# Kernel optimization log

Hardware: AMD Instinct MI355X
Metric: run time of the kernel (lower is better)

Reference implementation:

```python
import jax, jax.numpy as jnp
import numpy as np

EMBED = 1024
HEADS = 16
HEAD_DIM = EMBED // HEADS


def _rope(t):
    # t: (B, S, H, D) -> rotary embedding applied over last dim (GPT-NeoX rotate-half)
    B, S, H, D = t.shape
    half = D // 2
    inv_freq = 1.0 / (10000.0 ** (jnp.arange(0, half, dtype=jnp.float32) / half))
    freqs = jnp.arange(S, dtype=jnp.float32)[:, None] * inv_freq[None, :]  # (S, half)
    cos = jnp.cos(freqs)[None, :, None, :]
    sin = jnp.sin(freqs)[None, :, None, :]
    t1, t2 = t[..., :half], t[..., half:]
    return jnp.concatenate([t1 * cos - t2 * sin, t2 * cos + t1 * sin], axis=-1)


def setup_inputs() -> dict:
    key = jax.random.key(0)
    k1, k2, k3 = jax.random.split(key, 3)
    B, S = 2, 2048
    x = jax.random.normal(k1, (B, S, EMBED), dtype=jnp.float32)
    attn_mask = jnp.ones((B, S), dtype=bool)
    w_qkv = jax.random.normal(k2, (EMBED, 3 * EMBED), dtype=jnp.float32) * (1.0 / np.sqrt(EMBED))
    w_out = jax.random.normal(k3, (EMBED, EMBED), dtype=jnp.float32) * (1.0 / np.sqrt(EMBED))
    return {"x": x, "attn_mask": attn_mask, "w_qkv": w_qkv, "w_out": w_out, "is_causal": 1}


def reference(x, attn_mask, w_qkv, w_out, is_causal):
    B, S, E = x.shape
    qkv = x @ w_qkv                                   # (B, S, 3E)
    q, k, v = jnp.split(qkv, 3, axis=-1)
    q = q.reshape(B, S, HEADS, HEAD_DIM)
    k = k.reshape(B, S, HEADS, HEAD_DIM)
    v = v.reshape(B, S, HEADS, HEAD_DIM)
    q = _rope(q)
    k = _rope(k)
    scale = 1.0 / np.sqrt(HEAD_DIM)
    scores = jnp.einsum('bqhd,bkhd->bhqk', q, k) * scale  # (B, H, S, S)
    neg = jnp.asarray(-1e30, dtype=scores.dtype)
    if is_causal:
        causal = jnp.tril(jnp.ones((S, S), dtype=bool))
        scores = jnp.where(causal[None, None], scores, neg)
    else:
        scores = jnp.where(attn_mask[:, None, None, :], scores, neg)
    attn = jax.nn.softmax(scores, axis=-1)
    y = jnp.einsum('bhqk,bkhd->bqhd', attn, v).reshape(B, S, E)
    return y @ w_out
```

## Files before the change

kernel.cpp:

```cpp
#include <hip/hip_runtime.h>
#include <hip/hip_bf16.h>
#include <stdint.h>

typedef float v4f __attribute__((ext_vector_type(4)));
typedef short v8s __attribute__((ext_vector_type(8)));

#define LOG2E 1.44269504088896f
#define QSCALE (0.125f * LOG2E)
#define SOFTMAX_OFF 16.0f

__device__ __forceinline__ unsigned short f2bf(float f) {
    unsigned int u = __float_as_uint(f);
    u += 0x7fffu + ((u >> 16) & 1u);
    return (unsigned short)(u >> 16);
}

#define LDS_FENCE() __builtin_amdgcn_fence(__ATOMIC_ACQ_REL, "workgroup")

__device__ __forceinline__ void gload_lds16(const unsigned short* g, unsigned short* s) {
    __builtin_amdgcn_global_load_lds(
        (const __attribute__((address_space(1))) unsigned int*)g,
        (__attribute__((address_space(3))) unsigned int*)s, 16, 0, 0);
}

#define BAR()      asm volatile("s_barrier" ::: "memory")
#define VMWAIT(N)  asm volatile("s_waitcnt vmcnt(" #N ")" ::: "memory")

#define PIPE_BARRIER_KEEP4()                                   \
    do {                                                       \
        asm volatile("s_waitcnt vmcnt(4)" ::: "memory");       \
        __builtin_amdgcn_s_barrier();                          \
        asm volatile("" ::: "memory");                         \
    } while (0)
#define PIPE_BARRIER_DRAIN()                                   \
    do {                                                       \
        asm volatile("s_waitcnt vmcnt(0)" ::: "memory");       \
        __builtin_amdgcn_s_barrier();                          \
        asm volatile("" ::: "memory");                         \
    } while (0)

__global__ void k_prep(const float* __restrict__ x,
                       const float* __restrict__ w_qkv,
                       const float* __restrict__ w_out,
                       unsigned short* __restrict__ xb,
                       unsigned short* __restrict__ wqkvT,
                       unsigned short* __restrict__ woutT,
                       float2* __restrict__ rope) {
    __shared__ unsigned short tile[64][65];
    int id = blockIdx.x, t = threadIdx.x;
    if (id < 1024) {
        int base = id * 256 + t;
#pragma unroll
        for (int k = 0; k < 4; ++k) {
            int i = base + k * 262144;
            float4 v = ((const float4*)x)[i];
            ushort4 o;
            o.x = f2bf(v.x); o.y = f2bf(v.y); o.z = f2bf(v.z); o.w = f2bf(v.w);
            ((ushort4*)xb)[i] = o;
        }
        return;
    }
    id -= 1024;
    if (id < 256) {
        int idx = id * 256 + t;
        int s = idx >> 5, d = idx & 31;
        float inv = __expf(-(float)d * 0.28782313662425572f);
        float sn, cs;
        sincosf((float)s * inv, &sn, &cs);
        rope[idx] = make_float2(cs, sn);
        return;
    }
    id -= 256;
    const float* src; unsigned short* dst; int N, kb, nb;
    if (id < 768) { src = w_qkv; dst = wqkvT; N = 3072; nb = (id % 48) * 64; kb = (id / 48) * 64; }
    else { id -= 768; src = w_out; dst = woutT; N = 1024; nb = (id % 16) * 64; kb = (id / 16) * 64; }
    const int K = 1024;
    for (int i = 0; i < 16; ++i) {
        int e = t + i * 256;
        int n_l = e & 63, k_l = e >> 6;
        tile[n_l][k_l] = f2bf(src[(size_t)(kb + k_l) * N + nb + n_l]);
    }
    __syncthreads();
    for (int i = 0; i < 16; ++i) {
        int e = t + i * 256;
        int k_l = e & 63, n_l = e >> 6;
        dst[(size_t)(nb + n_l) * K + kb + k_l] = tile[n_l][k_l];
    }
}

__global__ __launch_bounds__(512, 2) void k_gemm_qkv(
    const unsigned short* __restrict__ A,
    const unsigned short* __restrict__ Bt,
    const float2* __restrict__ rope,
    unsigned short* __restrict__ Qg,
    unsigned short* __restrict__ Kg,
    unsigned short* __restrict__ Vt) {
    const int K = 1024;
    __shared__ __align__(16) union {
        struct { unsigned short Ab[2][256 * 64], Bb[2][256 * 64]; } g;
        unsigned short vt[4][64][264];
    } sm;
    const int t = threadIdx.x;
    const int w = t >> 6, l = t & 63, quad = l >> 4, ln = l & 15;
    const int wr = w >> 2, wc = w & 3;
    const int mb = blockIdx.y * 256, nb = blockIdx.x * 256;
    const int lxr = l >> 3;
    const int swz = ((l & 7) ^ lxr) * 8;

    v4f acc[8][4];
#pragma unroll
    for (int i = 0; i < 8; ++i)
#pragma unroll
        for (int j = 0; j < 4; ++j) acc[i][j] = (v4f){0.f, 0.f, 0.f, 0.f};

    auto stageHT = [&](const unsigned short* src, int grow, int k0, unsigned short* lds) {
#pragma unroll
        for (int c = 0; c < 2; ++c) {
            int r0 = w * 16 + c * 8;
            gload_lds16(src + (size_t)(grow + r0 + lxr) * K + k0 + swz, lds + r0 * 64);
        }
    };
    auto frag = [&](const unsigned short* base, int row, int g16) -> v8s {
        return *(const v8s*)&base[row * 64 + ((g16 ^ (row & 7)) << 3)];
    };

    stageHT(A,  mb,       0,  &sm.g.Ab[0][0]);
    stageHT(A,  mb + 128, 0,  &sm.g.Ab[0][128 * 64]);
    stageHT(Bt, nb,       0,  &sm.g.Bb[0][0]);
    stageHT(Bt, nb + 128, 0,  &sm.g.Bb[0][128 * 64]);
    stageHT(A,  mb,       64, &sm.g.Ab[1][0]);
    stageHT(A,  mb + 128, 64, &sm.g.Ab[1][128 * 64]);
    VMWAIT(4);
    BAR();

    for (int kt = 0; kt < 16; ++kt) {
        const int buf = kt & 1, nbf = buf ^ 1;
        const unsigned short* Ap = &sm.g.Ab[buf][0];
        const unsigned short* Bp = &sm.g.Bb[buf][0];
        if (kt + 1 < 16) stageHT(Bt, nb, (kt + 1) * 64, &sm.g.Bb[nbf][0]);
        v8s a0[8], b0[4];
#pragma unroll
        for (int i = 0; i < 8; ++i) a0[i] = frag(Ap, wr * 128 + i * 16 + ln, quad);
#pragma unroll
        for (int j = 0; j < 4; ++j) b0[j] = frag(Bp, wc * 64 + j * 16 + ln, quad);
        __builtin_amdgcn_s_setprio(1);
#pragma unroll
        for (int i = 0; i < 8; ++i) {
            acc[i][0] = __builtin_amdgcn_mfma_f32_16x16x32_bf16(a0[i], b0[0], acc[i][0], 0, 0, 0);
            acc[i][1] = __builtin_amdgcn_mfma_f32_16x16x32_bf16(a0[i], b0[1], acc[i][1], 0, 0, 0);
        }
        __builtin_amdgcn_s_setprio(0);
        BAR();
        if (kt + 1 < 16) stageHT(Bt, nb + 128, (kt + 1) * 64, &sm.g.Bb[nbf][128 * 64]);
        v8s a1[8], b1[4];
#pragma unroll
        for (int i = 0; i < 8; ++i) a1[i] = frag(Ap, wr * 128 + i * 16 + ln, 4 + quad);
#pragma unroll
        for (int j = 0; j < 4; ++j) b1[j] = frag(Bp, wc * 64 + j * 16 + ln, 4 + quad);
        __builtin_amdgcn_s_setprio(1);
#pragma unroll
        for (int i = 0; i < 8; ++i) {
            acc[i][2] = __builtin_amdgcn_mfma_f32_16x16x32_bf16(a0[i], b0[2], acc[i][2], 0, 0, 0);
            acc[i][3] = __builtin_amdgcn_mfma_f32_16x16x32_bf16(a0[i], b0[3], acc[i][3], 0, 0, 0);
        }
        __builtin_amdgcn_s_setprio(0);
        BAR();
        if (kt + 2 < 16) stageHT(A, mb, (kt + 2) * 64, &sm.g.Ab[buf][0]);
        __builtin_amdgcn_s_setprio(1);
#pragma unroll
        for (int i = 0; i < 8; ++i) {
            acc[i][0] = __builtin_amdgcn_mfma_f32_16x16x32_bf16(a1[i], b1[0], acc[i][0], 0, 0, 0);
            acc[i][1] = __builtin_amdgcn_mfma_f32_16x16x32_bf16(a1[i], b1[1], acc[i][1], 0, 0, 0);
        }
        __builtin_amdgcn_s_setprio(0);
        BAR();
        if (kt + 2 < 16) stageHT(A, mb + 128, (kt + 2) * 64, &sm.g.Ab[buf][128 * 64]);
        __builtin_amdgcn_s_setprio(1);
#pragma unroll
        for (int i = 0; i < 8; ++i) {
            acc[i][2] = __builtin_amdgcn_mfma_f32_16x16x32_bf16(a1[i], b1[2], acc[i][2], 0, 0, 0);
            acc[i][3] = __builtin_amdgcn_mfma_f32_16x16x32_bf16(a1[i], b1[3], acc[i][3], 0, 0, 0);
        }
        __builtin_amdgcn_s_setprio(0);
        if (kt < 14)       VMWAIT(4);
        else if (kt == 14) VMWAIT(0);
        if (kt < 15) BAR();
    }

    if (nb >= 2048) {
        __syncthreads();
#pragma unroll
        for (int i = 0; i < 8; ++i)
#pragma unroll
            for (int j = 0; j < 4; ++j) {
                int d = j * 16 + ln;
                int s0 = wr * 128 + i * 16 + quad * 4;
                ushort4 pk;
                pk.x = f2bf(acc[i][j][0]); pk.y = f2bf(acc[i][j][1]);
                pk.z = f2bf(acc[i][j][2]); pk.w = f2bf(acc[i][j][3]);
                *(ushort4*)&sm.vt[wc][d][s0] = pk;
            }
        __syncthreads();
        const int hbase = (nb & 1023) >> 6;
        const int b = mb >> 11, sbase = mb & 2047;
#pragma unroll
        for (int i = 0; i < 16; ++i) {
            int c = t + i * 512;
            int h2 = c >> 11, dd = (c >> 5) & 63, off = (c & 31) * 8;
            v8s val = *(const v8s*)&sm.vt[h2][dd][off];
            *(v8s*)(Vt + ((size_t)((b * 16 + hbase + h2) * 64 + dd) * 2048 + sbase + off)) = val;
        }
        return;
    }

    const int nbw = nb + wc * 64;
    const int region = nbw >> 10;
    const int h = (nbw & 1023) >> 6;
    unsigned short* dst = region == 0 ? Qg : Kg;
    const float scale = region == 0 ? QSCALE : 1.0f;
#pragma unroll
    for (int jj = 0; jj < 2; ++jj) {
        const float2* rp = rope + jj * 16 + ln;
#pragma unroll
        for (int i = 0; i < 8; ++i)
#pragma unroll
            for (int r = 0; r < 4; ++r) {
                int row = mb + wr * 128 + i * 16 + quad * 4 + r;
                int s = row & 2047, b = row >> 11;
                float2 cs = rp[s * 32];
                float t1 = acc[i][jj][r], t2 = acc[i][jj + 2][r];
                size_t base = ((size_t)(b * 16 + h) * 2048 + s) * 64;
                dst[base + jj * 16 + ln]      = f2bf((t1 * cs.x - t2 * cs.y) * scale);
                dst[base + jj * 16 + ln + 32] = f2bf((t2 * cs.x + t1 * cs.y) * scale);
            }
    }
}

__global__ __launch_bounds__(256) void k_gemm_out(
    const unsigned short* __restrict__ A,
    const unsigned short* __restrict__ Bt,
    float* __restrict__ C) {
    const int K = 1024, N = 1024;
    __shared__ __align__(16) unsigned short Ab[3][4096];
    __shared__ __align__(16) unsigned short Bb[3][4096];
    const int t = threadIdx.x;
    const int w = t >> 6, l = t & 63, quad = l >> 4, ln = l & 15;
    const int wm = (w >> 1) * 64, wn = (w & 1) * 64;
    const int mb = blockIdx.y * 128, nb = blockIdx.x * 128;

    v4f acc[4][4];
#pragma unroll
    for (int i = 0; i < 4; ++i)
#pragma unroll
        for (int j = 0; j < 4; ++j) acc[i][j] = (v4f){0.f, 0.f, 0.f, 0.f};

    auto stage = [&](int buf, int k0) {
#pragma unroll
        for (int u = 0; u < 2; ++u) {
            int e = t + u * 256;
            gload_lds16(A + (size_t)(mb + (e >> 2)) * K + k0 + (e & 3) * 8,
                        &Ab[buf][(w * 64 + u * 256) * 8]);
            gload_lds16(Bt + (size_t)(nb + (e >> 2)) * K + k0 + (e & 3) * 8,
                        &Bb[buf][(w * 64 + u * 256) * 8]);
        }
    };

    stage(0, 0);
    stage(1, 32);
    int cur = 0, nxt = 2;
    for (int itk = 0; itk < 32; ++itk) {
        if (itk < 31) PIPE_BARRIER_KEEP4();
        else          PIPE_BARRIER_DRAIN();
        if (itk + 2 < 32) {
            stage(nxt, (itk + 2) * 32);
            nxt = nxt == 2 ? 0 : nxt + 1;
        }
        v8s af[4], bfr[4];
#pragma unroll
        for (int i = 0; i < 4; ++i)
            af[i] = *(const v8s*)&Ab[cur][(wm + i * 16 + ln) * 32 + quad * 8];
#pragma unroll
        for (int j = 0; j < 4; ++j)
            bfr[j] = *(const v8s*)&Bb[cur][(wn + j * 16 + ln) * 32 + quad * 8];
#pragma unroll
        for (int i = 0; i < 4; ++i)
#pragma unroll
            for (int j = 0; j < 4; ++j)
                acc[i][j] = __builtin_amdgcn_mfma_f32_16x16x32_bf16(
                    af[i], bfr[j], acc[i][j], 0, 0, 0);
        cur = cur == 2 ? 0 : cur + 1;
    }

#pragma unroll
    for (int i = 0; i < 4; ++i) {
        int r0 = mb + wm + i * 16 + quad * 4;
#pragma unroll
        for (int j = 0; j < 4; ++j) {
            int c0 = nb + wn + j * 16 + ln;
#pragma unroll
            for (int r = 0; r < 4; ++r)
                C[(size_t)(r0 + r) * N + c0] = acc[i][j][r];
        }
    }
}

__global__ __launch_bounds__(256) void k_flash(
    const unsigned short* __restrict__ Qg,
    const unsigned short* __restrict__ Kg,
    const unsigned short* __restrict__ Vt,
    unsigned short* __restrict__ Og) {
    __shared__ __align__(16) unsigned short Kb[2][64 * 64];
    __shared__ __align__(16) unsigned short Vb[2][64 * 64];
    __shared__ __align__(16) unsigned short P[4][16][72];

    const int id = blockIdx.x;
    const int xcd = id & 7, slot = id >> 3;
    const int bh = xcd * 4 + (slot & 3);
    const int qt = 31 - (slot >> 2);
    const int qbase = qt * 64;
    const int nit = qt + 1;

    const int t = threadIdx.x, w = t >> 6, l = t & 63, quad = l >> 4, ln = l & 15;
    const int b = bh >> 4, h = bh & 15;

    const unsigned short* Qp = Qg + (size_t)bh * 2048 * 64;
    const unsigned short* Kp = Kg + (size_t)bh * 2048 * 64;
    const unsigned short* Vp = Vt + (size_t)bh * 64 * 2048;

    unsigned kst[2], vst[2];
    int cchunk = l & 7, rloc = l >> 3;
#pragma unroll
    for (int j = 0; j < 2; ++j) {
        int c = w + j * 4;
        int rr = c * 8 + rloc;
        int g = (cchunk + rr) & 7;
        kst[j] = (unsigned)(rr * 64 + g * 8);
        vst[j] = (unsigned)(rr * 2048 + g * 8);
    }
    const int c0 = ((quad - ln) & 7) * 8;
    const int c1 = ((quad + 4 - ln) & 7) * 8;
    const v8s ones = {0x3F80, 0x3F80, 0x3F80, 0x3F80, 0x3F80, 0x3F80, 0x3F80, 0x3F80};

    const int qrow = qbase + w * 16 + ln;
    v8s qf0 = *(const v8s*)(Qp + (size_t)qrow * 64 + quad * 8);
    v8s qf1 = *(const v8s*)(Qp + (size_t)qrow * 64 + quad * 8 + 32);

    v4f oacc[5];
#pragma unroll
    for (int dt = 0; dt < 5; ++dt) oacc[dt] = (v4f){0.f, 0.f, 0.f, 0.f};

    auto stage = [&](int buf, int kvb) {
        const unsigned short* kg = Kp + (size_t)kvb * 64;
        const unsigned short* vg = Vp + kvb;
#pragma unroll
        for (int j = 0; j < 2; ++j) {
            int c = w + j * 4;
            gload_lds16(kg + kst[j], &Kb[buf][c * 512]);
            gload_lds16(vg + vst[j], &Vb[buf][c * 512]);
        }
    };

    auto compute = [&](int buf, int it) {
        v4f sc[4];
#pragma unroll
        for (int kt = 0; kt < 4; ++kt) {
            int row = kt * 16 + ln;
            v8s k0 = *(const v8s*)&Kb[buf][row * 64 + c0];
            v8s k1 = *(const v8s*)&Kb[buf][row * 64 + c1];
            sc[kt] = (v4f){0.f, 0.f, 0.f, 0.f};
            sc[kt] = __builtin_amdgcn_mfma_f32_16x16x32_bf16(qf0, k0, sc[kt], 0, 0, 0);
            sc[kt] = __builtin_amdgcn_mfma_f32_16x16x32_bf16(qf1, k1, sc[kt], 0, 0, 0);
        }
        if (it == qt) {
            int q0 = qbase + w * 16 + quad * 4;
#pragma unroll
            for (int kt = 0; kt < 4; ++kt) {
                int kv = qbase + kt * 16 + ln;
#pragma unroll
                for (int r = 0; r < 4; ++r)
                    if (kv > q0 + r) sc[kt][r] = -1e30f;
            }
        }
#pragma unroll
        for (int kt = 0; kt < 4; ++kt)
#pragma unroll
            for (int r = 0; r < 4; ++r)
                sc[kt][r] = exp2f(sc[kt][r] - SOFTMAX_OFF);

#pragma unroll
        for (int kt = 0; kt < 4; ++kt) {
            union { __hip_bfloat162 hh; unsigned int u; } p01, p23;
            p01.hh = __float22bfloat162_rn(make_float2(sc[kt][0], sc[kt][1]));
            p23.hh = __float22bfloat162_rn(make_float2(sc[kt][2], sc[kt][3]));
            P[w][quad * 4 + 0][kt * 16 + ln] = (unsigned short)p01.u;
            P[w][quad * 4 + 1][kt * 16 + ln] = (unsigned short)(p01.u >> 16);
            P[w][quad * 4 + 2][kt * 16 + ln] = (unsigned short)p23.u;
            P[w][quad * 4 + 3][kt * 16 + ln] = (unsigned short)(p23.u >> 16);
        }
        LDS_FENCE();
        v8s pf0 = *(const v8s*)&P[w][ln][quad * 8];
        v8s pf1 = *(const v8s*)&P[w][ln][quad * 8 + 32];
        LDS_FENCE();
        __builtin_amdgcn_s_setprio(1);
#pragma unroll
        for (int dt = 0; dt < 4; ++dt) {
            int row = dt * 16 + ln;
            v8s v0 = *(const v8s*)&Vb[buf][row * 64 + c0];
            v8s v1 = *(const v8s*)&Vb[buf][row * 64 + c1];
            oacc[dt] = __builtin_amdgcn_mfma_f32_16x16x32_bf16(pf0, v0, oacc[dt], 0, 0, 0);
            oacc[dt] = __builtin_amdgcn_mfma_f32_16x16x32_bf16(pf1, v1, oacc[dt], 0, 0, 0);
        }
        oacc[4] = __builtin_amdgcn_mfma_f32_16x16x32_bf16(pf0, ones, oacc[4], 0, 0, 0);
        oacc[4] = __builtin_amdgcn_mfma_f32_16x16x32_bf16(pf1, ones, oacc[4], 0, 0, 0);
        __builtin_amdgcn_s_setprio(0);
    };

    stage(0, 0);
    for (int it = 0;;) {
        const int buf = it & 1;
        stage(buf ^ 1, (it + 1) * 64);
        VMWAIT(4);
        BAR();
        compute(buf, it);
        if (++it >= nit) break;
        BAR();
    }

    float rden[4];
#pragma unroll
    for (int r = 0; r < 4; ++r) rden[r] = 1.f / oacc[4][r];
#pragma unroll
    for (int dt = 0; dt < 4; ++dt)
#pragma unroll
        for (int r = 0; r < 4; ++r) {
            int s = qbase + w * 16 + quad * 4 + r;
            Og[(size_t)(b * 2048 + s) * 1024 + h * 64 + dt * 16 + ln] =
                f2bf(oacc[dt][r] * rden[r]);
        }
}

extern "C" void kernel_launch(void* const* d_in, const int* in_sizes, int n_in,
                              void* d_out, int out_size, void* d_ws, size_t ws_size,
                              hipStream_t stream) {
    const float* x     = (const float*)d_in[0];
    const float* w_qkv = (const float*)d_in[2];
    const float* w_out = (const float*)d_in[3];
    char* ws = (char*)d_ws;

    unsigned short* xb    = (unsigned short*)(ws);
    unsigned short* wqkvT = (unsigned short*)(ws + (size_t)(8 << 20));
    unsigned short* woutT = (unsigned short*)(ws + (size_t)(14 << 20));
    unsigned short* Qg    = (unsigned short*)(ws + (size_t)(16 << 20));
    unsigned short* Kg    = (unsigned short*)(ws + (size_t)(24 << 20));
    unsigned short* Vt    = (unsigned short*)(ws + (size_t)(32 << 20));
    unsigned short* Og    = (unsigned short*)(ws + (size_t)(40 << 20));
    float2*         rope  = (float2*)(ws + (size_t)(48 << 20));

    k_prep<<<2304, 256, 0, stream>>>(x, w_qkv, w_out, xb, wqkvT, woutT, rope);
    k_gemm_qkv<<<dim3(12, 16), 512, 0, stream>>>(xb, wqkvT, rope, Qg, Kg, Vt);
    k_flash<<<1024, 256, 0, stream>>>(Qg, Kg, Vt, Og);
    k_gemm_out<<<dim3(8, 32), 256, 0, stream>>>(Og, woutT, (float*)d_out);
}
```

Measured before the change: 196.5 us.

## Restructure QKV GEMM main loop into 8-phase quadrant schedule with explicit LDS waits

Rewrites the QKV projection GEMM K-loop into a two-tile-per-iteration schedule. Each tile's 256x256 output is split into four quadrants, and LDS fragment reads, global-to-LDS staging, barriers and MFMA blocks are interleaved in a fixed order with explicit lgkmcnt waits and sched_barriers. The prologue now preloads B for the second stage instead of A. The aim is to hold fewer fragment registers live and to overlap LDS reads and global loads with MFMA more tightly. The cost is more barriers per K step and a greater risk of buffer-reuse hazards.

```diff
diff --git a/kernel.cpp b/kernel.cpp
--- a/kernel.cpp
+++ b/kernel.cpp
@@ -25,6 +25,8 @@
 
 #define BAR()      asm volatile("s_barrier" ::: "memory")
 #define VMWAIT(N)  asm volatile("s_waitcnt vmcnt(" #N ")" ::: "memory")
+#define LGKM0()    do { asm volatile("s_waitcnt lgkmcnt(0)" ::: "memory"); \
+                        __builtin_amdgcn_sched_barrier(0); } while (0)
 
 #define PIPE_BARRIER_KEEP4()                                   \
     do {                                                       \
@@ -124,67 +126,94 @@
         return *(const v8s*)&base[row * 64 + ((g16 ^ (row & 7)) << 3)];
     };
 
+    v8s aF[4][2], bF0[2][2], bF1[2][2];
+    auto readA = [&](const unsigned short* Ap, int ih) {
+#pragma unroll
+        for (int ii = 0; ii < 4; ++ii) {
+            int row = wr * 128 + (ih * 4 + ii) * 16 + ln;
+#pragma unroll
+            for (int kh = 0; kh < 2; ++kh) aF[ii][kh] = frag(Ap, row, kh * 4 + quad);
+        }
+    };
+    auto readB = [&](const unsigned short* Bp, int jh, v8s (&bF)[2][2]) {
+#pragma unroll
+        for (int jj = 0; jj < 2; ++jj) {
+            int row = wc * 64 + (jh * 2 + jj) * 16 + ln;
+#pragma unroll
+            for (int kh = 0; kh < 2; ++kh) bF[jj][kh] = frag(Bp, row, kh * 4 + quad);
+        }
+    };
+    auto mfma16 = [&](v8s (&bF)[2][2], int ih, int jh) {
+        __builtin_amdgcn_s_setprio(1);
+#pragma unroll
+        for (int ii = 0; ii < 4; ++ii)
+#pragma unroll
+            for (int jj = 0; jj < 2; ++jj) {
+                v4f* ac = &acc[ih * 4 + ii][jh * 2 + jj];
+                *ac = __builtin_amdgcn_mfma_f32_16x16x32_bf16(aF[ii][0], bF[jj][0], *ac, 0, 0, 0);
+                *ac = __builtin_amdgcn_mfma_f32_16x16x32_bf16(aF[ii][1], bF[jj][1], *ac, 0, 0, 0);
+            }
+        __builtin_amdgcn_s_setprio(0);
+        __builtin_amdgcn_sched_barrier(0);
+    };
+
+    const unsigned short* Ap0 = &sm.g.Ab[0][0];
+    const unsigned short* Ap1 = &sm.g.Ab[1][0];
+    const unsigned short* Bp0 = &sm.g.Bb[0][0];
+    const unsigned short* Bp1 = &sm.g.Bb[1][0];
+
     stageHT(A,  mb,       0,  &sm.g.Ab[0][0]);
     stageHT(A,  mb + 128, 0,  &sm.g.Ab[0][128 * 64]);
     stageHT(Bt, nb,       0,  &sm.g.Bb[0][0]);
     stageHT(Bt, nb + 128, 0,  &sm.g.Bb[0][128 * 64]);
-    stageHT(A,  mb,       64, &sm.g.Ab[1][0]);
-    stageHT(A,  mb + 128, 64, &sm.g.Ab[1][128 * 64]);
+    stageHT(Bt, nb,       64, &sm.g.Bb[1][0]);
+    stageHT(Bt, nb + 128, 64, &sm.g.Bb[1][128 * 64]);
     VMWAIT(4);
     BAR();
 
-    for (int kt = 0; kt < 16; ++kt) {
-        const int buf = kt & 1, nbf = buf ^ 1;
-        const unsigned short* Ap = &sm.g.Ab[buf][0];
-        const unsigned short* Bp = &sm.g.Bb[buf][0];
-        if (kt + 1 < 16) stageHT(Bt, nb, (kt + 1) * 64, &sm.g.Bb[nbf][0]);
-        v8s a0[8], b0[4];
-#pragma unroll
-        for (int i = 0; i < 8; ++i) a0[i] = frag(Ap, wr * 128 + i * 16 + ln, quad);
-#pragma unroll
-        for (int j = 0; j < 4; ++j) b0[j] = frag(Bp, wc * 64 + j * 16 + ln, quad);
-        __builtin_amdgcn_s_setprio(1);
-#pragma unroll
-        for (int i = 0; i < 8; ++i) {
-            acc[i][0] = __builtin_amdgcn_mfma_f32_16x16x32_bf16(a0[i], b0[0], acc[i][0], 0, 0, 0);
-            acc[i][1] = __builtin_amdgcn_mfma_f32_16x16x32_bf16(a0[i], b0[1], acc[i][1], 0, 0, 0);
-        }
-        __builtin_amdgcn_s_setprio(0);
-        BAR();
-        if (kt + 1 < 16) stageHT(Bt, nb + 128, (kt + 1) * 64, &sm.g.Bb[nbf][128 * 64]);
-        v8s a1[8], b1[4];
-#pragma unroll
-        for (int i = 0; i < 8; ++i) a1[i] = frag(Ap, wr * 128 + i * 16 + ln, 4 + quad);
-#pragma unroll
-        for (int j = 0; j < 4; ++j) b1[j] = frag(Bp, wc * 64 + j * 16 + ln, 4 + quad);
-        __builtin_amdgcn_s_setprio(1);
-#pragma unroll
-        for (int i = 0; i < 8; ++i) {
-            acc[i][2] = __builtin_amdgcn_mfma_f32_16x16x32_bf16(a0[i], b0[2], acc[i][2], 0, 0, 0);
-            acc[i][3] = __builtin_amdgcn_mfma_f32_16x16x32_bf16(a0[i], b0[3], acc[i][3], 0, 0, 0);
-        }
-        __builtin_amdgcn_s_setprio(0);
-        BAR();
-        if (kt + 2 < 16) stageHT(A, mb, (kt + 2) * 64, &sm.g.Ab[buf][0]);
-        __builtin_amdgcn_s_setprio(1);
-#pragma unroll
-        for (int i = 0; i < 8; ++i) {
-            acc[i][0] = __builtin_amdgcn_mfma_f32_16x16x32_bf16(a1[i], b1[0], acc[i][0], 0, 0, 0);
-            acc[i][1] = __builtin_amdgcn_mfma_f32_16x16x32_bf16(a1[i], b1[1], acc[i][1], 0, 0, 0);
-        }
-        __builtin_amdgcn_s_setprio(0);
-        BAR();
-        if (kt + 2 < 16) stageHT(A, mb + 128, (kt + 2) * 64, &sm.g.Ab[buf][128 * 64]);
-        __builtin_amdgcn_s_setprio(1);
-#pragma unroll
-        for (int i = 0; i < 8; ++i) {
-            acc[i][2] = __builtin_amdgcn_mfma_f32_16x16x32_bf16(a1[i], b1[2], acc[i][2], 0, 0, 0);
-            acc[i][3] = __builtin_amdgcn_mfma_f32_16x16x32_bf16(a1[i], b1[3], acc[i][3], 0, 0, 0);
-        }
-        __builtin_amdgcn_s_setprio(0);
-        if (kt < 14)       VMWAIT(4);
-        else if (kt == 14) VMWAIT(0);
-        if (kt < 15) BAR();
+    for (int it = 0; it < 8; ++it) {
+        const int c1k = (2 * it + 1) * 64, n0k = (2 * it + 2) * 64, n1k = (2 * it + 3) * 64;
+        const bool pre = it < 7;
+        readA(Ap0, 0); readB(Bp0, 0, bF0);
+        stageHT(A, mb, c1k, &sm.g.Ab[1][0]);
+        BAR(); LGKM0();
+        mfma16(bF0, 0, 0);
+        BAR();
+        readB(Bp0, 1, bF1);
+        stageHT(A, mb + 128, c1k, &sm.g.Ab[1][128 * 64]);
+        BAR(); LGKM0();
+        mfma16(bF1, 0, 1);
+        BAR();
+        readA(Ap0, 1);
+        if (pre) stageHT(Bt, nb, n0k, &sm.g.Bb[0][0]);
+        BAR(); LGKM0();
+        mfma16(bF0, 1, 0);
+        BAR();
+        if (pre) stageHT(Bt, nb + 128, n0k, &sm.g.Bb[0][128 * 64]);
+        BAR();
+        mfma16(bF1, 1, 1);
+        if (pre) VMWAIT(4); else VMWAIT(0);
+        BAR();
+        readA(Ap1, 0); readB(Bp1, 0, bF0);
+        if (pre) stageHT(A, mb, n0k, &sm.g.Ab[0][0]);
+        BAR(); LGKM0();
+        mfma16(bF0, 0, 0);
+        BAR();
+        readB(Bp1, 1, bF1);
+        if (pre) stageHT(A, mb + 128, n0k, &sm.g.Ab[0][128 * 64]);
+        BAR(); LGKM0();
+        mfma16(bF1, 0, 1);
+        BAR();
+        readA(Ap1, 1);
+        if (pre) stageHT(Bt, nb, n1k, &sm.g.Bb[1][0]);
+        BAR(); LGKM0();
+        mfma16(bF0, 1, 0);
+        BAR();
+        if (pre) stageHT(Bt, nb + 128, n1k, &sm.g.Bb[1][128 * 64]);
+        BAR();
+        mfma16(bF1, 1, 1);
+        if (pre) VMWAIT(4);
+        BAR();
     }
 
     if (nb >= 2048) {
```

New measurement: 199.0 us. Within noise of the previous version (+1.3%).
